# Kernel tuning notes

Hardware: AMD Instinct MI355X
Metric: run time of the kernel (lower is better)

Reference implementation:

```python
import jax, jax.numpy as jnp
import numpy as np

EPS = 1e-6  # flax.linen.LayerNorm default

def layer_norm(x, scale, bias):
    mean = jnp.mean(x, axis=-1, keepdims=True)
    var = jnp.mean(jnp.square(x - mean), axis=-1, keepdims=True)
    return (x - mean) * jax.lax.rsqrt(var + EPS) * scale + bias

def setup_inputs() -> dict:
    key = jax.random.key(0)
    ks = jax.random.split(key, 4)
    B, P, D, H = 2, 2048, 768, 12
    hd = D // H
    x = jax.random.normal(ks[0], (B, P, D), dtype=jnp.float32)
    W_qkv = jax.random.normal(ks[1], (D, 3 * D), dtype=jnp.float32) * (D ** -0.5)
    W_out = jax.random.normal(ks[2], (D, D), dtype=jnp.float32) * (D ** -0.5)
    b_out = jnp.zeros((D,), dtype=jnp.float32)
    return {
        "x": x,
        "W_qkv": W_qkv,
        "q_scale": jnp.ones((hd,), jnp.float32),
        "q_bias": jnp.zeros((hd,), jnp.float32),
        "k_scale": jnp.ones((hd,), jnp.float32),
        "k_bias": jnp.zeros((hd,), jnp.float32),
        "o_scale": jnp.ones((D,), jnp.float32),
        "o_bias": jnp.zeros((D,), jnp.float32),
        "W_out": W_out,
        "b_out": b_out,
    }

def reference(x, W_qkv, q_scale, q_bias, k_scale, k_bias, o_scale, o_bias, W_out, b_out):
    B, P, D = x.shape
    H = 12
    hd = D // H
    scale = hd ** -0.5
    # fused QKV projection, no bias
    qkv = (x @ W_qkv).reshape(B, P, 3, H, hd).transpose(2, 0, 3, 1, 4)  # [3,B,H,P,hd]
    q, k, v = qkv[0], qkv[1], qkv[2]
    # per-head QK LayerNorm over head_dim
    q = layer_norm(q, q_scale, q_bias) * scale
    k = layer_norm(k, k_scale, k_bias)
    attn = jnp.einsum("bhqd,bhkd->bhqk", q, k)
    attn = jax.nn.softmax(attn, axis=-1)
    out = jnp.einsum("bhqk,bhkd->bhqd", attn, v)  # [B,H,P,hd]
    out = jnp.swapaxes(out, 1, 2).reshape(B, P, D)
    out = layer_norm(out, o_scale, o_bias)
    return out @ W_out + b_out
```

## Files before the change

### kernel.cpp

```cpp
#include <hip/hip_runtime.h>
#include <hip/hip_bf16.h>

#define B_  2
#define P_  2048
#define D_  768
#define H_  12
#define HD_ 64
#define M_  (B_ * P_)
#define N1_ (3 * D_)

typedef __attribute__((ext_vector_type(8))) short short8;
typedef __attribute__((ext_vector_type(4))) float f32x4;
typedef __attribute__((ext_vector_type(16))) float f32x16;
typedef __attribute__((ext_vector_type(4))) unsigned u32x4;
typedef unsigned short ushort;

__device__ __forceinline__ ushort f2bf(float f) {
    unsigned u = __float_as_uint(f);
    u += 0x7fffu + ((u >> 16) & 1u);
    return (ushort)(u >> 16);
}

__device__ __forceinline__ unsigned cvtpk(float a, float b) {
    unsigned r;
    asm("v_cvt_pk_bf16_f32 %0, %1, %2" : "=v"(r) : "v"(a), "v"(b));
    return r;
}

__device__ __forceinline__ int swap23(int s) {
    return (s & ~12) | ((s & 4) << 1) | ((s & 8) >> 1);
}

#define QSC_ (0.125f * 1.44269504088896340736f)

__global__ __launch_bounds__(512) void gemm_qkv_mfma(
        const float* __restrict__ x, const float* __restrict__ w,
        const float* __restrict__ qs, const float* __restrict__ qb,
        const float* __restrict__ ks, const float* __restrict__ kb,
        ushort* __restrict__ qkv) {
    __shared__ __align__(16) ushort As[128][40];
    __shared__ __align__(16) ushort Bs[128][40];

    const int tid  = threadIdx.x;
    const int lane = tid & 63;
    const int wv   = tid >> 6;
    const int quad = lane >> 4;
    const int col  = lane & 15;
    const int wr   = (wv >> 1) * 32;
    const int wc   = (wv & 1) * 64;
    const int rowBase = blockIdx.y * 128;
    const int colBase = blockIdx.x * 128;

    const int am0 = tid >> 3, ac4 = tid & 7;
    const int nB  = tid & 127, kq = tid >> 7;

    float4 apre[2];
    float  bpre[8];
    auto load_tile = [&](int kt) {
        const int k0 = kt * 32;
        apre[0] = *(const float4*)(x + (size_t)(rowBase + am0) * D_ + k0 + ac4 * 4);
        apre[1] = *(const float4*)(x + (size_t)(rowBase + am0 + 64) * D_ + k0 + ac4 * 4);
#pragma unroll
        for (int j = 0; j < 8; j++)
            bpre[j] = w[(size_t)(k0 + kq * 8 + j) * N1_ + colBase + nB];
    };

    f32x4 acc[2][4];
#pragma unroll
    for (int i = 0; i < 2; i++)
#pragma unroll
        for (int j = 0; j < 4; j++) acc[i][j] = (f32x4){0.f, 0.f, 0.f, 0.f};

    load_tile(0);
    const int NT = D_ / 32;
    for (int kt = 0; kt < NT; kt++) {
        __syncthreads();
        {
            uint2 a0 = {cvtpk(apre[0].x, apre[0].y), cvtpk(apre[0].z, apre[0].w)};
            uint2 a1 = {cvtpk(apre[1].x, apre[1].y), cvtpk(apre[1].z, apre[1].w)};
            *(uint2*)&As[am0][ac4 * 4]      = a0;
            *(uint2*)&As[am0 + 64][ac4 * 4] = a1;
            u32x4 bb;
#pragma unroll
            for (int j = 0; j < 4; j++) bb[j] = cvtpk(bpre[2 * j], bpre[2 * j + 1]);
            *(u32x4*)&Bs[nB][kq * 8] = bb;
        }
        __syncthreads();
        if (kt + 1 < NT) load_tile(kt + 1);

        short8 af[2], bf[4];
#pragma unroll
        for (int mt = 0; mt < 2; mt++) af[mt] = *(const short8*)&As[wr + mt * 16 + col][quad * 8];
#pragma unroll
        for (int nt = 0; nt < 4; nt++) bf[nt] = *(const short8*)&Bs[wc + nt * 16 + col][quad * 8];
#pragma unroll
        for (int mt = 0; mt < 2; mt++)
#pragma unroll
            for (int nt = 0; nt < 4; nt++)
                acc[mt][nt] = __builtin_amdgcn_mfma_f32_16x16x32_bf16(af[mt], bf[nt], acc[mt][nt], 0, 0, 0);
    }

    const int comp = colBase / D_;
    const int rem  = colBase + wc - comp * D_;
    const int h    = rem >> 6;
    float sc4[4] = {0, 0, 0, 0}, bi4[4] = {0, 0, 0, 0};
    if (comp == 0) {
#pragma unroll
        for (int nt = 0; nt < 4; nt++) { sc4[nt] = qs[nt * 16 + col]; bi4[nt] = qb[nt * 16 + col]; }
    } else if (comp == 1) {
#pragma unroll
        for (int nt = 0; nt < 4; nt++) { sc4[nt] = ks[nt * 16 + col]; bi4[nt] = kb[nt * 16 + col]; }
    }

#pragma unroll
    for (int mt = 0; mt < 2; mt++) {
#pragma unroll
        for (int r = 0; r < 4; r++) {
            int m  = rowBase + wr + mt * 16 + quad * 4 + r;
            int bb = m >> 11;
            int p  = m & 2047;
            float v0 = acc[mt][0][r], v1 = acc[mt][1][r], v2 = acc[mt][2][r], v3 = acc[mt][3][r];
            if (comp < 2) {
                float s = v0 + v1 + v2 + v3;
#pragma unroll
                for (int off = 1; off < 16; off <<= 1) s += __shfl_xor(s, off, 64);
                float mean = s * (1.0f / 64.0f);
                float d0 = v0 - mean, d1 = v1 - mean, d2 = v2 - mean, d3 = v3 - mean;
                float sq = d0 * d0 + d1 * d1 + d2 * d2 + d3 * d3;
#pragma unroll
                for (int off = 1; off < 16; off <<= 1) sq += __shfl_xor(sq, off, 64);
                float inv = rsqrtf(sq * (1.0f / 64.0f) + 1e-6f);
                v0 = d0 * inv * sc4[0] + bi4[0];
                v1 = d1 * inv * sc4[1] + bi4[1];
                v2 = d2 * inv * sc4[2] + bi4[2];
                v3 = d3 * inv * sc4[3] + bi4[3];
                if (comp == 0) { v0 *= QSC_; v1 *= QSC_; v2 *= QSC_; v3 *= QSC_; }
            }
            size_t base = ((((size_t)comp * B_ + bb) * H_ + h) * P_ + p) * HD_;
            qkv[base +  0 + col] = f2bf(v0);
            qkv[base + 16 + col] = f2bf(v1);
            qkv[base + 32 + col] = f2bf(v2);
            qkv[base + 48 + col] = f2bf(v3);
        }
    }
}

__global__ __launch_bounds__(256) void attn_split(const ushort* __restrict__ qkv,
                                                  float* __restrict__ o0, float* __restrict__ o1,
                                                  float* __restrict__ o2, float* __restrict__ o3,
                                                  float* __restrict__ l0, float* __restrict__ l1,
                                                  float* __restrict__ l2, float* __restrict__ l3) {
    const int p0  = blockIdx.x * 128;
    const int bh  = blockIdx.y;
    const int s   = blockIdx.z;
    const int nsp = gridDim.z;
    const int b   = bh / H_, h = bh % H_;
    float* opart = (s == 0) ? o0 : (s == 1) ? o1 : (s == 2) ? o2 : o3;
    float* lpart = (s == 0) ? l0 : (s == 1) ? l1 : (s == 2) ? l2 : l3;
    const int tid  = threadIdx.x;
    const int lane = tid & 63;
    const int wv   = tid >> 6;
    const int half = lane >> 5;
    const int n32  = lane & 31;

    __shared__ __align__(16) ushort KVs[2][2][64][72];

    const size_t hs  = (size_t)P_ * HD_;
    const int    kv0 = s * (P_ / nsp);
    const ushort* qg = qkv + ((size_t)(0 * B_ + b) * H_ + h) * hs + (size_t)(p0 + wv * 32) * HD_;
    const ushort* kg = qkv + ((size_t)(1 * B_ + b) * H_ + h) * hs + (size_t)kv0 * HD_;
    const ushort* vg = qkv + ((size_t)(2 * B_ + b) * H_ + h) * hs + (size_t)kv0 * HD_;

    short8 aq[4];
#pragma unroll
    for (int ks2 = 0; ks2 < 4; ks2++)
        aq[ks2] = *(const short8*)(qg + (size_t)n32 * HD_ + ks2 * 16 + half * 8);

    float lsum = 0.f;
    f32x16 oaccT[2];
#pragma unroll
    for (int nt = 0; nt < 2; nt++)
#pragma unroll
        for (int r = 0; r < 16; r++) oaccT[nt][r] = 0.f;

    const int kr = tid >> 3, kc8 = tid & 7;
    const int krs = swap23(kr);
    const int vd = tid & 63,  vkh = tid >> 6;

    uint4  kpre[2];
    ushort vpre[16];
    auto load_tile = [&](int kt) {
        const ushort* kg_t = kg + (size_t)kt * 64 * HD_;
        const ushort* vg_t = vg + (size_t)kt * 64 * HD_;
        kpre[0] = *(const uint4*)(kg_t + (size_t)kr * HD_ + kc8 * 8);
        kpre[1] = *(const uint4*)(kg_t + (size_t)(kr + 32) * HD_ + kc8 * 8);
#pragma unroll
        for (int j = 0; j < 16; j++)
            vpre[j] = vg_t[(size_t)(vkh * 16 + j) * HD_ + vd];
    };
    auto stage = [&](int buf) {
        *(uint4*)&KVs[buf][0][krs][kc8 * 8]      = kpre[0];
        *(uint4*)&KVs[buf][0][krs + 32][kc8 * 8] = kpre[1];
        *(short8*)&KVs[buf][1][vd][vkh * 16]     = *(short8*)&vpre[0];
        *(short8*)&KVs[buf][1][vd][vkh * 16 + 8] = *(short8*)&vpre[8];
    };

    load_tile(0);
    stage(0);
    __syncthreads();

    const int NT = (P_ / 64) / nsp;
    int cur = 0;
    for (int kt = 0; kt < NT; kt++) {
        const bool more = (kt + 1 < NT);
        if (more) load_tile(kt + 1);

        ushort (*Ks)[72] = KVs[cur][0];
        ushort (*Vs)[72] = KVs[cur][1];

#pragma unroll
        for (int nt = 0; nt < 2; nt++) {
            f32x16 sc;
#pragma unroll
            for (int r = 0; r < 16; r++) sc[r] = 0.f;
#pragma unroll
            for (int ks2 = 0; ks2 < 4; ks2++) {
                short8 kb2 = *(const short8*)&Ks[nt * 32 + n32][ks2 * 16 + half * 8];
                sc = __builtin_amdgcn_mfma_f32_32x32x16_bf16(kb2, aq[ks2], sc, 0, 0, 0);
            }
            float p[16];
#pragma unroll
            for (int r = 0; r < 16; r++) {
                p[r] = __builtin_amdgcn_exp2f(sc[r]);
                lsum += p[r];
            }
            unsigned w[8];
#pragma unroll
            for (int i = 0; i < 8; i++) w[i] = cvtpk(p[2 * i], p[2 * i + 1]);
#pragma unroll
            for (int kp2 = 0; kp2 < 2; kp2++) {
                u32x4 t = {w[kp2 * 4 + 0], w[kp2 * 4 + 1], w[kp2 * 4 + 2], w[kp2 * 4 + 3]};
                short8 pb = __builtin_bit_cast(short8, t);
                const int kstep = nt * 2 + kp2;
#pragma unroll
                for (int ntd = 0; ntd < 2; ntd++) {
                    short8 av = *(const short8*)&Vs[ntd * 32 + n32][kstep * 16 + half * 8];
                    oaccT[ntd] = __builtin_amdgcn_mfma_f32_32x32x16_bf16(av, pb, oaccT[ntd], 0, 0, 0);
                }
            }
        }

        if (more) {
            stage(cur ^ 1);
            __syncthreads();
            cur ^= 1;
        }
    }

    lsum += __shfl_xor(lsum, 32, 64);
    if (lane < 32)
        lpart[(size_t)bh * P_ + p0 + wv * 32 + lane] = lsum;

    float* scr = (float*)&KVs[0][0][0][0] + wv * 1152;
#pragma unroll
    for (int ntd = 0; ntd < 2; ntd++) {
#pragma unroll
        for (int r = 0; r < 16; r++)
            scr[n32 * 36 + (r & 3) + 8 * (r >> 2) + 4 * half] = oaccT[ntd][r];
#pragma unroll
        for (int i = 0; i < 4; i++) {
            int ql = i * 8 + (lane >> 3);
            int c4 = lane & 7;
            float4 v = *(const float4*)&scr[ql * 36 + c4 * 4];
            *(float4*)(opart + ((size_t)bh * P_ + p0 + wv * 32 + ql) * HD_ + ntd * 32 + c4 * 4) = v;
        }
    }
}

__global__ __launch_bounds__(256) void ln_o(const float* __restrict__ o0,
                                            const float* __restrict__ o1,
                                            const float* __restrict__ o2,
                                            const float* __restrict__ o3,
                                            const float* __restrict__ l0,
                                            const float* __restrict__ l1,
                                            const float* __restrict__ l2,
                                            const float* __restrict__ l3,
                                            const int ns,
                                            ushort* __restrict__ lnb,
                                            const float* __restrict__ osc,
                                            const float* __restrict__ ob) {
    __shared__ float red[4];
    __shared__ float red2[4];
    const int row = blockIdx.x;
    const int b   = row >> 11;
    const int p   = row & (P_ - 1);
    const int tid = threadIdx.x;

    auto src = [&](int d) {
        int h = d >> 6;
        size_t lr  = (size_t)(b * H_ + h) * P_ + p;
        size_t idx = lr * HD_ + (d & 63);
        float num = o0[idx] + o1[idx];
        float den = l0[lr] + l1[lr];
        if (ns == 4) { num += o2[idx] + o3[idx]; den += l2[lr] + l3[lr]; }
        return num / den;
    };
    float v0 = src(tid);
    float v1 = src(tid + 256);
    float v2 = src(tid + 512);
    float s = v0 + v1 + v2;
#pragma unroll
    for (int o = 32; o > 0; o >>= 1) s += __shfl_xor(s, o, 64);
    if ((tid & 63) == 0) red[tid >> 6] = s;
    __syncthreads();
    float mean = (red[0] + red[1] + red[2] + red[3]) * (1.0f / 768.0f);
    float d0 = v0 - mean, d1 = v1 - mean, d2 = v2 - mean;
    float sq = d0 * d0 + d1 * d1 + d2 * d2;
#pragma unroll
    for (int o = 32; o > 0; o >>= 1) sq += __shfl_xor(sq, o, 64);
    if ((tid & 63) == 0) red2[tid >> 6] = sq;
    __syncthreads();
    float var = (red2[0] + red2[1] + red2[2] + red2[3]) * (1.0f / 768.0f);
    float inv = rsqrtf(var + 1e-6f);
    const size_t base = (size_t)row * D_;
    lnb[base + tid]       = f2bf(d0 * inv * osc[tid]       + ob[tid]);
    lnb[base + tid + 256] = f2bf(d1 * inv * osc[tid + 256] + ob[tid + 256]);
    lnb[base + tid + 512] = f2bf(d2 * inv * osc[tid + 512] + ob[tid + 512]);
}

__global__ __launch_bounds__(256) void gemm_out_mfma(
        const ushort* __restrict__ a, const float* __restrict__ w,
        const float* __restrict__ bias, float* __restrict__ out) {
    __shared__ __align__(16) ushort As[64][40];
    __shared__ __align__(16) ushort Bs[64][40];

    const int tid  = threadIdx.x;
    const int lane = tid & 63;
    const int wv   = tid >> 6;
    const int quad = lane >> 4;
    const int col  = lane & 15;
    const int wr   = (wv >> 1) * 32;
    const int wc   = (wv & 1) * 32;
    const int rowBase = blockIdx.y * 64;
    const int colBase = blockIdx.x * 64;

    const int am  = tid >> 2, ac8 = tid & 3;
    const int nB  = tid & 63, kq = tid >> 6;

    uint4 apre;
    float bpre[8];
    auto load_tile = [&](int kt) {
        const int k0 = kt * 32;
        apre = *(const uint4*)(a + (size_t)(rowBase + am) * D_ + k0 + ac8 * 8);
#pragma unroll
        for (int j = 0; j < 8; j++)
            bpre[j] = w[(size_t)(k0 + kq * 8 + j) * D_ + colBase + nB];
    };

    f32x4 acc[2][2];
#pragma unroll
    for (int i = 0; i < 2; i++)
#pragma unroll
        for (int j = 0; j < 2; j++) acc[i][j] = (f32x4){0.f, 0.f, 0.f, 0.f};

    load_tile(0);
    const int NT = D_ / 32;
    for (int kt = 0; kt < NT; kt++) {
        __syncthreads();
        *(uint4*)&As[am][ac8 * 8] = apre;
        {
            u32x4 bb;
#pragma unroll
            for (int j = 0; j < 4; j++) bb[j] = cvtpk(bpre[2 * j], bpre[2 * j + 1]);
            *(u32x4*)&Bs[nB][kq * 8] = bb;
        }
        __syncthreads();
        if (kt + 1 < NT) load_tile(kt + 1);

        short8 af[2], bf[2];
#pragma unroll
        for (int mt = 0; mt < 2; mt++) af[mt] = *(const short8*)&As[wr + mt * 16 + col][quad * 8];
#pragma unroll
        for (int nt = 0; nt < 2; nt++) bf[nt] = *(const short8*)&Bs[wc + nt * 16 + col][quad * 8];
#pragma unroll
        for (int mt = 0; mt < 2; mt++)
#pragma unroll
            for (int nt = 0; nt < 2; nt++)
                acc[mt][nt] = __builtin_amdgcn_mfma_f32_16x16x32_bf16(af[mt], bf[nt], acc[mt][nt], 0, 0, 0);
    }

    float b2[2];
#pragma unroll
    for (int nt = 0; nt < 2; nt++) b2[nt] = bias[colBase + wc + nt * 16 + col];
#pragma unroll
    for (int mt = 0; mt < 2; mt++) {
#pragma unroll
        for (int r = 0; r < 4; r++) {
            int m = rowBase + wr + mt * 16 + quad * 4 + r;
            float* dst = out + (size_t)m * D_ + colBase + wc;
#pragma unroll
            for (int nt = 0; nt < 2; nt++)
                dst[nt * 16 + col] = acc[mt][nt][r] + b2[nt];
        }
    }
}

extern "C" void kernel_launch(void* const* d_in, const int* in_sizes, int n_in,
                              void* d_out, int out_size, void* d_ws, size_t ws_size,
                              hipStream_t stream) {
    const float* x    = (const float*)d_in[0];
    const float* Wqkv = (const float*)d_in[1];
    const float* qs   = (const float*)d_in[2];
    const float* qb   = (const float*)d_in[3];
    const float* ks   = (const float*)d_in[4];
    const float* kb   = (const float*)d_in[5];
    const float* osc  = (const float*)d_in[6];
    const float* ob   = (const float*)d_in[7];
    const float* Wout = (const float*)d_in[8];
    const float* bout = (const float*)d_in[9];
    float* out = (float*)d_out;

    ushort* qkv = (ushort*)d_ws;
    const size_t qkvE = (size_t)3 * B_ * H_ * P_ * HD_;
    const size_t oE   = (size_t)B_ * H_ * P_ * HD_;
    const size_t lE   = (size_t)B_ * H_ * P_;
    float* base = (float*)(qkv + qkvE);
    const size_t need4 = qkvE * sizeof(ushort) + (3 * oE + 4 * lE) * sizeof(float);
    const int nsp = (ws_size >= need4) ? 4 : 2;
    float* op[4];
    float* lbase;
    if (nsp == 4) {
        op[0] = base; op[1] = base + oE; op[2] = base + 2 * oE; op[3] = out;
        lbase = base + 3 * oE;
    } else {
        op[0] = base; op[1] = out; op[2] = base; op[3] = base;
        lbase = base + oE;
    }
    float* lp[4] = {lbase, lbase + lE, lbase + 2 * lE, lbase + 3 * lE};
    ushort* ln_buf = qkv;

    gemm_qkv_mfma<<<dim3(N1_ / 128, M_ / 128), 512, 0, stream>>>(x, Wqkv, qs, qb, ks, kb, qkv);
    attn_split<<<dim3(P_ / 128, B_ * H_, nsp), 256, 0, stream>>>(
        qkv, op[0], op[1], op[2], op[3], lp[0], lp[1], lp[2], lp[3]);
    ln_o<<<dim3(M_), 256, 0, stream>>>(
        op[0], op[1], op[2], op[3], lp[0], lp[1], lp[2], lp[3], nsp, ln_buf, osc, ob);
    gemm_out_mfma<<<dim3(D_ / 64, M_ / 64), 256, 0, stream>>>(ln_buf, Wout, bout, out);
}
```

Baseline: 199.3 us.

## Double-buffer GEMM LDS tiles and store attention partials as bf16

Both GEMM kernels now keep two LDS buffers, so each K step needs one barrier instead of two and the next tile is staged while the current one is consumed. The split-KV attention partial outputs are written as bf16 instead of fp32, and ln_o converts them back. This halves the traffic for the intermediate partial-sum buffers at the cost of extra LDS and bf16 rounding of the unnormalized partial sums before they are combined.

```diff
diff --git a/kernel.cpp b/kernel.cpp
--- a/kernel.cpp
+++ b/kernel.cpp
@@ -27,6 +27,10 @@
     return r;
 }
 
+__device__ __forceinline__ float bf2f(ushort u) {
+    return __uint_as_float((unsigned)u << 16);
+}
+
 __device__ __forceinline__ int swap23(int s) {
     return (s & ~12) | ((s & 4) << 1) | ((s & 8) >> 1);
 }
@@ -38,8 +42,8 @@
         const float* __restrict__ qs, const float* __restrict__ qb,
         const float* __restrict__ ks, const float* __restrict__ kb,
         ushort* __restrict__ qkv) {
-    __shared__ __align__(16) ushort As[128][40];
-    __shared__ __align__(16) ushort Bs[128][40];
+    __shared__ __align__(16) ushort As[2][128][40];
+    __shared__ __align__(16) ushort Bs[2][128][40];
 
     const int tid  = threadIdx.x;
     const int lane = tid & 63;
@@ -64,6 +68,16 @@
         for (int j = 0; j < 8; j++)
             bpre[j] = w[(size_t)(k0 + kq * 8 + j) * N1_ + colBase + nB];
     };
+    auto stage = [&](int buf) {
+        uint2 a0 = {cvtpk(apre[0].x, apre[0].y), cvtpk(apre[0].z, apre[0].w)};
+        uint2 a1 = {cvtpk(apre[1].x, apre[1].y), cvtpk(apre[1].z, apre[1].w)};
+        *(uint2*)&As[buf][am0][ac4 * 4]      = a0;
+        *(uint2*)&As[buf][am0 + 64][ac4 * 4] = a1;
+        u32x4 bb;
+#pragma unroll
+        for (int j = 0; j < 4; j++) bb[j] = cvtpk(bpre[2 * j], bpre[2 * j + 1]);
+        *(u32x4*)&Bs[buf][nB][kq * 8] = bb;
+    };
 
     f32x4 acc[2][4];
 #pragma unroll
@@ -72,32 +86,31 @@
         for (int j = 0; j < 4; j++) acc[i][j] = (f32x4){0.f, 0.f, 0.f, 0.f};
 
     load_tile(0);
+    stage(0);
+    __syncthreads();
+
     const int NT = D_ / 32;
+    int cur = 0;
     for (int kt = 0; kt < NT; kt++) {
-        __syncthreads();
-        {
-            uint2 a0 = {cvtpk(apre[0].x, apre[0].y), cvtpk(apre[0].z, apre[0].w)};
-            uint2 a1 = {cvtpk(apre[1].x, apre[1].y), cvtpk(apre[1].z, apre[1].w)};
-            *(uint2*)&As[am0][ac4 * 4]      = a0;
-            *(uint2*)&As[am0 + 64][ac4 * 4] = a1;
-            u32x4 bb;
-#pragma unroll
-            for (int j = 0; j < 4; j++) bb[j] = cvtpk(bpre[2 * j], bpre[2 * j + 1]);
-            *(u32x4*)&Bs[nB][kq * 8] = bb;
-        }
-        __syncthreads();
-        if (kt + 1 < NT) load_tile(kt + 1);
+        const bool more = (kt + 1 < NT);
+        if (more) load_tile(kt + 1);
 
         short8 af[2], bf[4];
 #pragma unroll
-        for (int mt = 0; mt < 2; mt++) af[mt] = *(const short8*)&As[wr + mt * 16 + col][quad * 8];
-#pragma unroll
-        for (int nt = 0; nt < 4; nt++) bf[nt] = *(const short8*)&Bs[wc + nt * 16 + col][quad * 8];
+        for (int mt = 0; mt < 2; mt++) af[mt] = *(const short8*)&As[cur][wr + mt * 16 + col][quad * 8];
+#pragma unroll
+        for (int nt = 0; nt < 4; nt++) bf[nt] = *(const short8*)&Bs[cur][wc + nt * 16 + col][quad * 8];
 #pragma unroll
         for (int mt = 0; mt < 2; mt++)
 #pragma unroll
             for (int nt = 0; nt < 4; nt++)
                 acc[mt][nt] = __builtin_amdgcn_mfma_f32_16x16x32_bf16(af[mt], bf[nt], acc[mt][nt], 0, 0, 0);
+
+        if (more) {
+            stage(cur ^ 1);
+            __syncthreads();
+            cur ^= 1;
+        }
     }
 
     const int comp = colBase / D_;
@@ -146,8 +159,8 @@
 }
 
 __global__ __launch_bounds__(256) void attn_split(const ushort* __restrict__ qkv,
-                                                  float* __restrict__ o0, float* __restrict__ o1,
-                                                  float* __restrict__ o2, float* __restrict__ o3,
+                                                  ushort* __restrict__ o0, ushort* __restrict__ o1,
+                                                  ushort* __restrict__ o2, ushort* __restrict__ o3,
                                                   float* __restrict__ l0, float* __restrict__ l1,
                                                   float* __restrict__ l2, float* __restrict__ l3) {
     const int p0  = blockIdx.x * 128;
@@ -155,8 +168,8 @@
     const int s   = blockIdx.z;
     const int nsp = gridDim.z;
     const int b   = bh / H_, h = bh % H_;
-    float* opart = (s == 0) ? o0 : (s == 1) ? o1 : (s == 2) ? o2 : o3;
-    float* lpart = (s == 0) ? l0 : (s == 1) ? l1 : (s == 2) ? l2 : l3;
+    ushort* opart = (s == 0) ? o0 : (s == 1) ? o1 : (s == 2) ? o2 : o3;
+    float*  lpart = (s == 0) ? l0 : (s == 1) ? l1 : (s == 2) ? l2 : l3;
     const int tid  = threadIdx.x;
     const int lane = tid & 63;
     const int wv   = tid >> 6;
@@ -272,15 +285,16 @@
             int ql = i * 8 + (lane >> 3);
             int c4 = lane & 7;
             float4 v = *(const float4*)&scr[ql * 36 + c4 * 4];
-            *(float4*)(opart + ((size_t)bh * P_ + p0 + wv * 32 + ql) * HD_ + ntd * 32 + c4 * 4) = v;
-        }
-    }
-}
-
-__global__ __launch_bounds__(256) void ln_o(const float* __restrict__ o0,
-                                            const float* __restrict__ o1,
-                                            const float* __restrict__ o2,
-                                            const float* __restrict__ o3,
+            uint2 pk = {cvtpk(v.x, v.y), cvtpk(v.z, v.w)};
+            *(uint2*)(opart + ((size_t)bh * P_ + p0 + wv * 32 + ql) * HD_ + ntd * 32 + c4 * 4) = pk;
+        }
+    }
+}
+
+__global__ __launch_bounds__(256) void ln_o(const ushort* __restrict__ o0,
+                                            const ushort* __restrict__ o1,
+                                            const ushort* __restrict__ o2,
+                                            const ushort* __restrict__ o3,
                                             const float* __restrict__ l0,
                                             const float* __restrict__ l1,
                                             const float* __restrict__ l2,
@@ -300,9 +314,9 @@
         int h = d >> 6;
         size_t lr  = (size_t)(b * H_ + h) * P_ + p;
         size_t idx = lr * HD_ + (d & 63);
-        float num = o0[idx] + o1[idx];
+        float num = bf2f(o0[idx]) + bf2f(o1[idx]);
         float den = l0[lr] + l1[lr];
-        if (ns == 4) { num += o2[idx] + o3[idx]; den += l2[lr] + l3[lr]; }
+        if (ns == 4) { num += bf2f(o2[idx]) + bf2f(o3[idx]); den += l2[lr] + l3[lr]; }
         return num / den;
     };
     float v0 = src(tid);
@@ -331,8 +345,8 @@
 __global__ __launch_bounds__(256) void gemm_out_mfma(
         const ushort* __restrict__ a, const float* __restrict__ w,
         const float* __restrict__ bias, float* __restrict__ out) {
-    __shared__ __align__(16) ushort As[64][40];
-    __shared__ __align__(16) ushort Bs[64][40];
+    __shared__ __align__(16) ushort As[2][64][40];
+    __shared__ __align__(16) ushort Bs[2][64][40];
 
     const int tid  = threadIdx.x;
     const int lane = tid & 63;
@@ -356,6 +370,13 @@
         for (int j = 0; j < 8; j++)
             bpre[j] = w[(size_t)(k0 + kq * 8 + j) * D_ + colBase + nB];
     };
+    auto stage = [&](int buf) {
+        *(uint4*)&As[buf][am][ac8 * 8] = apre;
+        u32x4 bb;
+#pragma unroll
+        for (int j = 0; j < 4; j++) bb[j] = cvtpk(bpre[2 * j], bpre[2 * j + 1]);
+        *(u32x4*)&Bs[buf][nB][kq * 8] = bb;
+    };
 
     f32x4 acc[2][2];
 #pragma unroll
@@ -364,29 +385,31 @@
         for (int j = 0; j < 2; j++) acc[i][j] = (f32x4){0.f, 0.f, 0.f, 0.f};
 
     load_tile(0);
+    stage(0);
+    __syncthreads();
+
     const int NT = D_ / 32;
+    int cur = 0;
     for (int kt = 0; kt < NT; kt++) {
-        __syncthreads();
-        *(uint4*)&As[am][ac8 * 8] = apre;
-        {
-            u32x4 bb;
-#pragma unroll
-            for (int j = 0; j < 4; j++) bb[j] = cvtpk(bpre[2 * j], bpre[2 * j + 1]);
-            *(u32x4*)&Bs[nB][kq * 8] = bb;
-        }
-        __syncthreads();
-        if (kt + 1 < NT) load_tile(kt + 1);
+        const bool more = (kt + 1 < NT);
+        if (more) load_tile(kt + 1);
 
         short8 af[2], bf[2];
 #pragma unroll
-        for (int mt = 0; mt < 2; mt++) af[mt] = *(const short8*)&As[wr + mt * 16 + col][quad * 8];
-#pragma unroll
-        for (int nt = 0; nt < 2; nt++) bf[nt] = *(const short8*)&Bs[wc + nt * 16 + col][quad * 8];
+        for (int mt = 0; mt < 2; mt++) af[mt] = *(const short8*)&As[cur][wr + mt * 16 + col][quad * 8];
+#pragma unroll
+        for (int nt = 0; nt < 2; nt++) bf[nt] = *(const short8*)&Bs[cur][wc + nt * 16 + col][quad * 8];
 #pragma unroll
         for (int mt = 0; mt < 2; mt++)
 #pragma unroll
             for (int nt = 0; nt < 2; nt++)
                 acc[mt][nt] = __builtin_amdgcn_mfma_f32_16x16x32_bf16(af[mt], bf[nt], acc[mt][nt], 0, 0, 0);
+
+        if (more) {
+            stage(cur ^ 1);
+            __syncthreads();
+            cur ^= 1;
+        }
     }
 
     float b2[2];
@@ -424,17 +447,17 @@
     const size_t qkvE = (size_t)3 * B_ * H_ * P_ * HD_;
     const size_t oE   = (size_t)B_ * H_ * P_ * HD_;
     const size_t lE   = (size_t)B_ * H_ * P_;
-    float* base = (float*)(qkv + qkvE);
-    const size_t need4 = qkvE * sizeof(ushort) + (3 * oE + 4 * lE) * sizeof(float);
+    ushort* obase = qkv + qkvE;
+    const size_t need4 = (qkvE + 3 * oE) * sizeof(ushort) + 4 * lE * sizeof(float);
     const int nsp = (ws_size >= need4) ? 4 : 2;
-    float* op[4];
+    ushort* op[4];
     float* lbase;
     if (nsp == 4) {
-        op[0] = base; op[1] = base + oE; op[2] = base + 2 * oE; op[3] = out;
-        lbase = base + 3 * oE;
+        op[0] = obase; op[1] = obase + oE; op[2] = obase + 2 * oE; op[3] = (ushort*)out;
+        lbase = (float*)(obase + 3 * oE);
     } else {
-        op[0] = base; op[1] = out; op[2] = base; op[3] = base;
-        lbase = base + oE;
+        op[0] = obase; op[1] = (ushort*)out; op[2] = obase; op[3] = obase;
+        lbase = (float*)(obase + oE);
     }
     float* lp[4] = {lbase, lbase + lE, lbase + 2 * lE, lbase + 3 * lE};
     ushort* ln_buf = qkv;
```

Result: slower. 207.6 us (+4.2%).
